# Kernel optimization log

Measured on AMD Instinct MI355X. Metric: run time of the kernel, lower is better.

The kernel has to match this reference:

```python
import jax, jax.numpy as jnp
import numpy as np

HIDDEN = 1024
HEADS = 16
HEAD_DIM = HIDDEN // HEADS


def setup_inputs() -> dict:
    key = jax.random.key(0)
    ks = jax.random.split(key, 4)
    B, S, H = 2, 2048, HIDDEN
    scale = 1.0 / np.sqrt(H)
    return {
        "inputs": jax.random.normal(ks[0], (B, S, H), dtype=jnp.float32),
        "mask": jnp.ones((B, S), dtype=jnp.int32),
        "Wq": jax.random.normal(ks[1], (H, H), dtype=jnp.float32) * scale,
        "bq": jnp.zeros((H,), dtype=jnp.float32),
        "Wk": jax.random.normal(ks[2], (H, H), dtype=jnp.float32) * scale,
        "bk": jnp.zeros((H,), dtype=jnp.float32),
        "Wv": jax.random.normal(ks[3], (H, H), dtype=jnp.float32) * scale,
        "bv": jnp.zeros((H,), dtype=jnp.float32),
    }


def _split_heads(x, B, S):
    # [B,S,H] -> [B,heads,S,head_dim]
    return x.reshape(B, S, HEADS, HEAD_DIM).transpose(0, 2, 1, 3)


def reference(inputs, mask, Wq, bq, Wk, bk, Wv, bv):
    B, S, H = inputs.shape
    q = _split_heads(inputs @ Wq.T + bq, B, S)
    k = _split_heads(inputs @ Wk.T + bk, B, S)
    v = _split_heads(inputs @ Wv.T + bv, B, S)
    scores = jnp.einsum("bhqd,bhkd->bhqk", q, k) / jnp.sqrt(
        jnp.asarray(HEAD_DIM, dtype=inputs.dtype))
    # mask broadcast [B,1,1,S]; zeros -> -inf
    scores = jnp.where(mask[:, None, None, :] == 0, -jnp.inf, scores)
    attn = jax.nn.softmax(scores, axis=-1)
    context = jnp.einsum("bhqk,bhkd->bhqd", attn, v)
    return context.transpose(0, 2, 1, 3).reshape(B, S, H)
```

## Files before the change

kernel.cpp:

```cpp
#include <hip/hip_runtime.h>
#include <hip/hip_fp16.h>

constexpr int S_LEN  = 2048;
constexpr int HID    = 1024;
constexpr int HEADS  = 16;
constexpr int HDIM   = 64;
constexpr int BATCH  = 2;
constexpr int BH     = BATCH * HEADS;
constexpr int M_ROWS = BATCH * S_LEN;

typedef _Float16 half8  __attribute__((ext_vector_type(8)));
typedef _Float16 half4v __attribute__((ext_vector_type(4)));
typedef _Float16 half2v __attribute__((ext_vector_type(2)));
typedef float    f32x4  __attribute__((ext_vector_type(4)));

constexpr float EXP2_OFF = -11.541560327111707f;
constexpr float Q_SCALE  = 0.18033688011112042f;

__global__ __launch_bounds__(256) void cvt_kernel(
    const float* __restrict__ X,  const float* __restrict__ Wq,
    const float* __restrict__ Wk, const float* __restrict__ Wv,
    const int* __restrict__ mask,
    _Float16* __restrict__ Xh,  _Float16* __restrict__ Wqh,
    _Float16* __restrict__ Wkh, _Float16* __restrict__ Wvh,
    float* __restrict__ maskF)
{
    const int blk = blockIdx.x;
    if (blk >= 3584) {
        const int loc = blk - 3584;
        const size_t e = ((size_t)loc * 256 + threadIdx.x) * 8;
        #pragma unroll
        for (int i = 0; i < 8; ++i)
            maskF[e + i] = mask[e + i] ? EXP2_OFF : -1.0e30f;
        return;
    }
    const float* src; _Float16* dst; int loc;
    if (blk < 2048)      { src = X;  dst = Xh;  loc = blk; }
    else if (blk < 2560) { src = Wq; dst = Wqh; loc = blk - 2048; }
    else if (blk < 3072) { src = Wk; dst = Wkh; loc = blk - 2560; }
    else                 { src = Wv; dst = Wvh; loc = blk - 3072; }
    const size_t e = ((size_t)loc * 256 + threadIdx.x) * 8;
    float4 a = *reinterpret_cast<const float4*>(&src[e]);
    float4 b = *reinterpret_cast<const float4*>(&src[e + 4]);
    half8 h = { (_Float16)a.x, (_Float16)a.y, (_Float16)a.z, (_Float16)a.w,
                (_Float16)b.x, (_Float16)b.y, (_Float16)b.z, (_Float16)b.w };
    *reinterpret_cast<half8*>(&dst[e]) = h;
}

__device__ __forceinline__ void async_cp16(_Float16* lds, const _Float16* g) {
    __builtin_amdgcn_global_load_lds(
        (const __attribute__((address_space(1))) void*)g,
        (__attribute__((address_space(3))) void*)lds, 16, 0, 0);
}

__global__ __launch_bounds__(256) void qkv_proj_kernel(
    const _Float16* __restrict__ Xh,
    const _Float16* __restrict__ Wqh, const _Float16* __restrict__ Wkh,
    const _Float16* __restrict__ Wvh,
    const float* __restrict__ bq, const float* __restrict__ bk,
    const float* __restrict__ bv,
    _Float16* __restrict__ Qo, _Float16* __restrict__ Ko,
    _Float16* __restrict__ Vt)
{
    const int mode = blockIdx.z;
    const _Float16* W    = (mode == 0) ? Wqh : (mode == 1) ? Wkh : Wvh;
    const float*    bias = (mode == 0) ? bq  : (mode == 1) ? bk  : bv;

    const int m0 = blockIdx.x * 128, n0 = blockIdx.y * 128;
    const int tid = threadIdx.x, wave = tid >> 6, lane = tid & 63;
    const int l15 = lane & 15, quad = lane >> 4;

    __shared__ _Float16 SMEM[18432];
    _Float16* As = SMEM;
    _Float16* Bs = SMEM + 8192;

    f32x4 acc[4][4];
    #pragma unroll
    for (int mt = 0; mt < 4; ++mt)
        #pragma unroll
        for (int nt = 0; nt < 4; ++nt) acc[mt][nt] = (f32x4){0.f, 0.f, 0.f, 0.f};

    const int wm = (wave & 1) * 64, wn = (wave >> 1) * 64;

    for (int k0 = 0; k0 < HID; k0 += 64) {
        #pragma unroll
        for (int i = 0; i < 4; ++i) {
            const int chunk = wave * 4 + i;
            const int row   = chunk * 8 + (lane >> 3);
            const int lofs  = chunk * 512 + lane * 8;
            const int scol  = (lane & 7) * 8;
            async_cp16(&As[lofs], &Xh[(size_t)(m0 + row) * HID + k0 + scol]);
            async_cp16(&Bs[lofs], &W [(size_t)(n0 + row) * HID + k0 + scol]);
        }
        __syncthreads();

        #pragma unroll
        for (int c = 0; c < 2; ++c) {
            half8 af[4], bf[4];
            #pragma unroll
            for (int mt = 0; mt < 4; ++mt)
                af[mt] = *reinterpret_cast<const half8*>(
                    &As[(wm + mt * 16 + l15) * 64 + c * 32 + quad * 8]);
            #pragma unroll
            for (int nt = 0; nt < 4; ++nt)
                bf[nt] = *reinterpret_cast<const half8*>(
                    &Bs[(wn + nt * 16 + l15) * 64 + c * 32 + quad * 8]);
            #pragma unroll
            for (int mt = 0; mt < 4; ++mt)
                #pragma unroll
                for (int nt = 0; nt < 4; ++nt)
                    acc[mt][nt] = __builtin_amdgcn_mfma_f32_16x16x32_f16(
                        af[mt], bf[nt], acc[mt][nt], 0, 0, 0);
        }
        __syncthreads();
    }
    _Float16* T = SMEM + wave * 4608;

    const int nn  = n0 + wn;
    const int hh  = nn >> 6;
    const int mm  = m0 + wm;
    const int bb  = mm >> 11;
    const int bhv = bb * HEADS + hh;
    const int s0  = mm & 2047;
    const int rowg = lane >> 3, chunk = lane & 7;

    if (mode < 2) {
        _Float16* Out = (mode == 0) ? Qo : Ko;
        #pragma unroll
        for (int nt = 0; nt < 4; ++nt) {
            const int col = nt * 16 + l15;
            float bias_n = bias[nn + col];
            #pragma unroll
            for (int mt = 0; mt < 4; ++mt)
                #pragma unroll
                for (int r = 0; r < 4; ++r) {
                    float v = acc[mt][nt][r] + bias_n;
                    if (mode == 0) v *= Q_SCALE;
                    T[(mt * 16 + quad * 4 + r) * 72 + col] = (_Float16)v;
                }
        }
        asm volatile("s_waitcnt lgkmcnt(0)" ::: "memory");
        #pragma unroll
        for (int j = 0; j < 8; ++j) {
            const int srow = j * 8 + rowg;
            half8 v = *reinterpret_cast<const half8*>(&T[srow * 72 + chunk * 8]);
            *reinterpret_cast<half8*>(
                &Out[((size_t)bhv * S_LEN + s0 + srow) * HDIM + chunk * 8]) = v;
        }
    } else {
        #pragma unroll
        for (int nt = 0; nt < 4; ++nt) {
            const int col = nt * 16 + l15;
            const float bias_n = bias[nn + col];
            #pragma unroll
            for (int mt = 0; mt < 4; ++mt) {
                half4v t = { (_Float16)(acc[mt][nt][0] + bias_n),
                             (_Float16)(acc[mt][nt][1] + bias_n),
                             (_Float16)(acc[mt][nt][2] + bias_n),
                             (_Float16)(acc[mt][nt][3] + bias_n) };
                *reinterpret_cast<half4v*>(&T[col * 72 + mt * 16 + quad * 4]) = t;
            }
        }
        asm volatile("s_waitcnt lgkmcnt(0)" ::: "memory");
        #pragma unroll
        for (int j = 0; j < 8; ++j) {
            const int drow = j * 8 + rowg;
            half8 v = *reinterpret_cast<const half8*>(&T[drow * 72 + chunk * 8]);
            *reinterpret_cast<half8*>(
                &Vt[((size_t)bhv * HDIM + drow) * S_LEN + s0 + chunk * 8]) = v;
        }
    }
}

__global__ __launch_bounds__(512) void attn_kernel(
    const _Float16* __restrict__ Q, const _Float16* __restrict__ K,
    const _Float16* __restrict__ Vt, const float* __restrict__ maskF,
    float* __restrict__ Out)
{
    const int id    = blockIdx.x;
    const int xcd   = id & 7, local = id >> 3;
    const int bh    = xcd * 4 + (local & 3);
    const int qt    = local >> 2;
    const int b = bh >> 4, h = bh & 15;
    const int tid = threadIdx.x, wave = tid >> 6, lane = tid & 63;
    const int l15 = lane & 15, quad = lane >> 4;

    __shared__ _Float16 Ks[2][64 * 64];
    __shared__ _Float16 Vs[2][64 * 64];
    __shared__ _Float16 Ps[8][16][68];

    const _Float16* Qb = Q  + (size_t)bh * S_LEN * HDIM;
    const _Float16* Kb = K  + (size_t)bh * S_LEN * HDIM;
    const _Float16* Vb = Vt + (size_t)bh * HDIM * S_LEN;
    const float*    mb = maskF + b * S_LEN;

    const int qrow = qt * 128 + wave * 16 + l15;
    half8 qf[2];
    qf[0] = *reinterpret_cast<const half8*>(&Qb[(size_t)qrow * HDIM + quad * 8]);
    qf[1] = *reinterpret_cast<const half8*>(&Qb[(size_t)qrow * HDIM + 32 + quad * 8]);

    f32x4 acc[4];
    #pragma unroll
    for (int mt = 0; mt < 4; ++mt) acc[mt] = (f32x4){0.f, 0.f, 0.f, 0.f};
    float den = 0.f;

    const int srow_t  = tid >> 3;
    const int schunk  = (tid & 7) ^ (srow_t & 7);
    auto stage = [&](int kb, int buf) {
        async_cp16(&Ks[buf][tid * 8],
                   &Kb[(size_t)(kb + srow_t) * HDIM + schunk * 8]);
        async_cp16(&Vs[buf][tid * 8],
                   &Vb[(size_t)srow_t * S_LEN + kb + schunk * 8]);
    };

    stage(0, 0);
    int buf = 0;
    const int rsw = (l15 & 7);

    for (int kb = 0; kb < S_LEN; kb += 64) {
        __syncthreads();
        if (kb + 64 < S_LEN) stage(kb + 64, buf ^ 1);

        float4 m4[4];
        #pragma unroll
        for (int nt = 0; nt < 4; ++nt)
            m4[nt] = *reinterpret_cast<const float4*>(&mb[kb + nt * 16 + quad * 4]);

        half8 kf[2][4];
        #pragma unroll
        for (int c = 0; c < 2; ++c)
            #pragma unroll
            for (int nt = 0; nt < 4; ++nt)
                kf[c][nt] = *reinterpret_cast<const half8*>(
                    &Ks[buf][(nt * 16 + l15) * 64 + ((c * 4 + quad) ^ rsw) * 8]);
        f32x4 sc[4];
        #pragma unroll
        for (int nt = 0; nt < 4; ++nt) sc[nt] = (f32x4){0.f, 0.f, 0.f, 0.f};
        #pragma unroll
        for (int c = 0; c < 2; ++c)
            #pragma unroll
            for (int nt = 0; nt < 4; ++nt)
                sc[nt] = __builtin_amdgcn_mfma_f32_16x16x32_f16(
                    kf[c][nt], qf[c], sc[nt], 0, 0, 0);

        half8 vf[2][4];
        #pragma unroll
        for (int c = 0; c < 2; ++c)
            #pragma unroll
            for (int mt = 0; mt < 4; ++mt)
                vf[c][mt] = *reinterpret_cast<const half8*>(
                    &Vs[buf][(mt * 16 + l15) * 64 + ((c * 4 + quad) ^ rsw) * 8]);

        #pragma unroll
        for (int nt = 0; nt < 4; ++nt) {
            float p0 = __builtin_amdgcn_exp2f(sc[nt][0] + m4[nt].x);
            float p1 = __builtin_amdgcn_exp2f(sc[nt][1] + m4[nt].y);
            float p2 = __builtin_amdgcn_exp2f(sc[nt][2] + m4[nt].z);
            float p3 = __builtin_amdgcn_exp2f(sc[nt][3] + m4[nt].w);
            den += (p0 + p1) + (p2 + p3);
            half2v lo = __builtin_bit_cast(half2v, __builtin_amdgcn_cvt_pkrtz(p0, p1));
            half2v hi = __builtin_bit_cast(half2v, __builtin_amdgcn_cvt_pkrtz(p2, p3));
            half4v pk = { lo[0], lo[1], hi[0], hi[1] };
            *reinterpret_cast<half4v*>(&Ps[wave][l15][nt * 16 + quad * 4]) = pk;
        }
        asm volatile("s_waitcnt lgkmcnt(0)" ::: "memory");

        #pragma unroll
        for (int c = 0; c < 2; ++c) {
            half4v plo = *reinterpret_cast<const half4v*>(
                &Ps[wave][l15][c * 32 + quad * 8]);
            half4v phi = *reinterpret_cast<const half4v*>(
                &Ps[wave][l15][c * 32 + quad * 8 + 4]);
            half8 pf = { plo[0], plo[1], plo[2], plo[3],
                         phi[0], phi[1], phi[2], phi[3] };
            #pragma unroll
            for (int mt = 0; mt < 4; ++mt)
                acc[mt] = __builtin_amdgcn_mfma_f32_16x16x32_f16(
                    vf[c][mt], pf, acc[mt], 0, 0, 0);
        }
        buf ^= 1;
    }

    den += __shfl_xor(den, 16, 64);
    den += __shfl_xor(den, 32, 64);
    const float inv = 1.0f / den;

    float* orow = Out + ((size_t)(b * S_LEN + qrow)) * HID + h * HDIM;
    #pragma unroll
    for (int mt = 0; mt < 4; ++mt) {
        float4 o = { acc[mt][0] * inv, acc[mt][1] * inv,
                     acc[mt][2] * inv, acc[mt][3] * inv };
        *reinterpret_cast<float4*>(&orow[mt * 16 + quad * 4]) = o;
    }
}

extern "C" void kernel_launch(void* const* d_in, const int* in_sizes, int n_in,
                              void* d_out, int out_size, void* d_ws, size_t ws_size,
                              hipStream_t stream) {
    const float* X  = (const float*)d_in[0];
    const int*   mk = (const int*)  d_in[1];
    const float* Wq = (const float*)d_in[2];
    const float* bq = (const float*)d_in[3];
    const float* Wk = (const float*)d_in[4];
    const float* bk = (const float*)d_in[5];
    const float* Wv = (const float*)d_in[6];
    const float* bv = (const float*)d_in[7];
    float* out = (float*)d_out;

    _Float16* Xh  = (_Float16*)d_ws;
    _Float16* Wqh = Xh  + (size_t)M_ROWS * HID;
    _Float16* Wkh = Wqh + (size_t)HID * HID;
    _Float16* Wvh = Wkh + (size_t)HID * HID;
    _Float16* Q   = Wvh + (size_t)HID * HID;
    _Float16* K   = Q   + (size_t)BH * S_LEN * HDIM;
    _Float16* Vt  = K   + (size_t)BH * S_LEN * HDIM;
    float*    maskF = (float*)(Vt + (size_t)BH * S_LEN * HDIM);

    cvt_kernel<<<3586, 256, 0, stream>>>(X, Wq, Wk, Wv, mk, Xh, Wqh, Wkh, Wvh, maskF);

    dim3 gp(M_ROWS / 128, HID / 128, 3);
    qkv_proj_kernel<<<gp, 256, 0, stream>>>(Xh, Wqh, Wkh, Wvh, bq, bk, bv, Q, K, Vt);

    attn_kernel<<<512, 512, 0, stream>>>(Q, K, Vt, maskF, out);
}
```

Measured before the change: 182.7 us.

## Use 32x32 MFMA with double-buffered swizzled LDS in QKV projection

Rewrites the QKV projection GEMM main loop to use 32x32x16 MFMA tiles instead of 16x16x32, with a K-step of 32. LDS staging is double-buffered, so the next K slice is fetched asynchronously while the current one is computed, and only one barrier is needed per iteration. The LDS layout uses an XOR swizzle to avoid bank conflicts. The epilogue is remapped to the 32x32 accumulator layout. This trades more loop iterations and barriers for better overlap and fewer LDS reads per MFMA.

```diff
diff --git a/kernel.cpp b/kernel.cpp
--- a/kernel.cpp
+++ b/kernel.cpp
@@ -13,6 +13,7 @@
 typedef _Float16 half4v __attribute__((ext_vector_type(4)));
 typedef _Float16 half2v __attribute__((ext_vector_type(2)));
 typedef float    f32x4  __attribute__((ext_vector_type(4)));
+typedef float    f32x16 __attribute__((ext_vector_type(16)));
 
 constexpr float EXP2_OFF = -11.541560327111707f;
 constexpr float Q_SCALE  = 0.18033688011112042f;
@@ -68,52 +69,71 @@
 
     const int m0 = blockIdx.x * 128, n0 = blockIdx.y * 128;
     const int tid = threadIdx.x, wave = tid >> 6, lane = tid & 63;
-    const int l15 = lane & 15, quad = lane >> 4;
+    const int l31 = lane & 31, kg = lane >> 5;
 
     __shared__ _Float16 SMEM[18432];
-    _Float16* As = SMEM;
-    _Float16* Bs = SMEM + 8192;
-
-    f32x4 acc[4][4];
+
+    f32x16 acc[2][2];
     #pragma unroll
-    for (int mt = 0; mt < 4; ++mt)
-        #pragma unroll
-        for (int nt = 0; nt < 4; ++nt) acc[mt][nt] = (f32x4){0.f, 0.f, 0.f, 0.f};
+    for (int mt = 0; mt < 2; ++mt)
+        #pragma unroll
+        for (int nt = 0; nt < 2; ++nt)
+            #pragma unroll
+            for (int i = 0; i < 16; ++i) acc[mt][nt][i] = 0.f;
 
     const int wm = (wave & 1) * 64, wn = (wave >> 1) * 64;
 
-    for (int k0 = 0; k0 < HID; k0 += 64) {
-        #pragma unroll
-        for (int i = 0; i < 4; ++i) {
-            const int chunk = wave * 4 + i;
-            const int row   = chunk * 8 + (lane >> 3);
-            const int lofs  = chunk * 512 + lane * 8;
-            const int scol  = (lane & 7) * 8;
-            async_cp16(&As[lofs], &Xh[(size_t)(m0 + row) * HID + k0 + scol]);
-            async_cp16(&Bs[lofs], &W [(size_t)(n0 + row) * HID + k0 + scol]);
-        }
+    const int srow = tid >> 2, spos = tid & 3;
+    auto stage = [&](int k0, int b) {
+        _Float16* Asb = SMEM + b * 8192;
+        _Float16* Bsb = Asb + 4096;
+        #pragma unroll
+        for (int j = 0; j < 2; ++j) {
+            const int row = srow + j * 64;
+            const int sch = spos ^ (row & 3);
+            async_cp16(&Asb[j * 2048 + tid * 8],
+                       &Xh[(size_t)(m0 + row) * HID + k0 + sch * 8]);
+            async_cp16(&Bsb[j * 2048 + tid * 8],
+                       &W [(size_t)(n0 + row) * HID + k0 + sch * 8]);
+        }
+    };
+
+    stage(0, 0);
+    int buf = 0;
+
+    for (int k0 = 0; k0 < HID; k0 += 32) {
         __syncthreads();
+        if (k0 + 32 < HID) stage(k0 + 32, buf ^ 1);
+        _Float16* Asb = SMEM + buf * 8192;
+        _Float16* Bsb = Asb + 4096;
 
         #pragma unroll
         for (int c = 0; c < 2; ++c) {
-            half8 af[4], bf[4];
-            #pragma unroll
-            for (int mt = 0; mt < 4; ++mt)
+            const int k8 = c * 2 + kg;
+            half8 af[2], bf[2];
+            #pragma unroll
+            for (int mt = 0; mt < 2; ++mt) {
+                const int row = wm + mt * 32 + l31;
                 af[mt] = *reinterpret_cast<const half8*>(
-                    &As[(wm + mt * 16 + l15) * 64 + c * 32 + quad * 8]);
-            #pragma unroll
-            for (int nt = 0; nt < 4; ++nt)
+                    &Asb[row * 32 + ((k8 ^ (row & 3)) * 8)]);
+            }
+            #pragma unroll
+            for (int nt = 0; nt < 2; ++nt) {
+                const int row = wn + nt * 32 + l31;
                 bf[nt] = *reinterpret_cast<const half8*>(
-                    &Bs[(wn + nt * 16 + l15) * 64 + c * 32 + quad * 8]);
-            #pragma unroll
-            for (int mt = 0; mt < 4; ++mt)
+                    &Bsb[row * 32 + ((k8 ^ (row & 3)) * 8)]);
+            }
+            #pragma unroll
+            for (int mt = 0; mt < 2; ++mt)
                 #pragma unroll
-                for (int nt = 0; nt < 4; ++nt)
-                    acc[mt][nt] = __builtin_amdgcn_mfma_f32_16x16x32_f16(
+                for (int nt = 0; nt < 2; ++nt)
+                    acc[mt][nt] = __builtin_amdgcn_mfma_f32_32x32x16_f16(
                         af[mt], bf[nt], acc[mt][nt], 0, 0, 0);
         }
-        __syncthreads();
-    }
+        buf ^= 1;
+    }
+    __syncthreads();
+
     _Float16* T = SMEM + wave * 4608;
 
     const int nn  = n0 + wn;
@@ -127,47 +147,51 @@
     if (mode < 2) {
         _Float16* Out = (mode == 0) ? Qo : Ko;
         #pragma unroll
-        for (int nt = 0; nt < 4; ++nt) {
-            const int col = nt * 16 + l15;
+        for (int nt = 0; nt < 2; ++nt) {
+            const int col = nt * 32 + l31;
             float bias_n = bias[nn + col];
             #pragma unroll
-            for (int mt = 0; mt < 4; ++mt)
+            for (int mt = 0; mt < 2; ++mt)
                 #pragma unroll
-                for (int r = 0; r < 4; ++r) {
+                for (int r = 0; r < 16; ++r) {
+                    const int row_l = (r & 3) + 8 * (r >> 2) + 4 * kg;
                     float v = acc[mt][nt][r] + bias_n;
                     if (mode == 0) v *= Q_SCALE;
-                    T[(mt * 16 + quad * 4 + r) * 72 + col] = (_Float16)v;
+                    T[(mt * 32 + row_l) * 72 + col] = (_Float16)v;
                 }
         }
         asm volatile("s_waitcnt lgkmcnt(0)" ::: "memory");
         #pragma unroll
         for (int j = 0; j < 8; ++j) {
-            const int srow = j * 8 + rowg;
-            half8 v = *reinterpret_cast<const half8*>(&T[srow * 72 + chunk * 8]);
+            const int sr = j * 8 + rowg;
+            half8 v = *reinterpret_cast<const half8*>(&T[sr * 72 + chunk * 8]);
             *reinterpret_cast<half8*>(
-                &Out[((size_t)bhv * S_LEN + s0 + srow) * HDIM + chunk * 8]) = v;
+                &Out[((size_t)bhv * S_LEN + s0 + sr) * HDIM + chunk * 8]) = v;
         }
     } else {
         #pragma unroll
-        for (int nt = 0; nt < 4; ++nt) {
-            const int col = nt * 16 + l15;
+        for (int nt = 0; nt < 2; ++nt) {
+            const int col = nt * 32 + l31;
             const float bias_n = bias[nn + col];
             #pragma unroll
-            for (int mt = 0; mt < 4; ++mt) {
-                half4v t = { (_Float16)(acc[mt][nt][0] + bias_n),
-                             (_Float16)(acc[mt][nt][1] + bias_n),
-                             (_Float16)(acc[mt][nt][2] + bias_n),
-                             (_Float16)(acc[mt][nt][3] + bias_n) };
-                *reinterpret_cast<half4v*>(&T[col * 72 + mt * 16 + quad * 4]) = t;
-            }
+            for (int mt = 0; mt < 2; ++mt)
+                #pragma unroll
+                for (int rg = 0; rg < 4; ++rg) {
+                    half4v t = { (_Float16)(acc[mt][nt][rg * 4 + 0] + bias_n),
+                                 (_Float16)(acc[mt][nt][rg * 4 + 1] + bias_n),
+                                 (_Float16)(acc[mt][nt][rg * 4 + 2] + bias_n),
+                                 (_Float16)(acc[mt][nt][rg * 4 + 3] + bias_n) };
+                    const int s_off = mt * 32 + 8 * rg + 4 * kg;
+                    *reinterpret_cast<half4v*>(&T[col * 72 + s_off]) = t;
+                }
         }
         asm volatile("s_waitcnt lgkmcnt(0)" ::: "memory");
         #pragma unroll
         for (int j = 0; j < 8; ++j) {
-            const int drow = j * 8 + rowg;
-            half8 v = *reinterpret_cast<const half8*>(&T[drow * 72 + chunk * 8]);
+            const int dr = j * 8 + rowg;
+            half8 v = *reinterpret_cast<const half8*>(&T[dr * 72 + chunk * 8]);
             *reinterpret_cast<half8*>(
-                &Vt[((size_t)bhv * HDIM + drow) * S_LEN + s0 + chunk * 8]) = v;
+                &Vt[((size_t)bhv * HDIM + dr) * S_LEN + s0 + chunk * 8]) = v;
         }
     }
 }
```

After: 173.6 us. -5.0%, faster.
